# Optimization experiments

Measured on AMD Instinct MI355X. Metric: run time of the kernel, lower is better.

## Reference

```python
import jax, jax.numpy as jnp
import numpy as np

N, E, G = 400000, 2500000, 512
IN_F, H, C = 7, 32, 2
EPS = 1e-5


def setup_inputs() -> dict:
    key = jax.random.key(0)
    ks = jax.random.split(key, 12)
    x = jax.random.normal(ks[0], (N, IN_F), jnp.float32)
    edge_index = jax.random.randint(ks[1], (2, E), 0, N, dtype=jnp.int64)
    edge_attr = jax.random.uniform(ks[2], (E,), jnp.float32)
    batch = jnp.sort(jax.random.randint(ks[3], (N,), 0, G, dtype=jnp.int64))

    def lin(k, i, o):
        return (jax.random.normal(k, (i, o), jnp.float32) / np.sqrt(i)).astype(jnp.float32)

    params = dict(
        W0=lin(ks[4], IN_F, H), b0=jnp.zeros((H,), jnp.float32),
        W1=lin(ks[5], H, H),    b1=jnp.zeros((H,), jnp.float32),
        W2=lin(ks[6], H, H),    b2=jnp.zeros((H,), jnp.float32),
        W3=lin(ks[7], H, H),    b3=jnp.zeros((H,), jnp.float32),
        bn_g=jnp.ones((3, H), jnp.float32), bn_b=jnp.zeros((3, H), jnp.float32),
        Wm0=lin(ks[8], H, H),   bm0=jnp.zeros((H,), jnp.float32),
        bnm_g=jnp.ones((H,), jnp.float32), bnm_b=jnp.zeros((H,), jnp.float32),
        Wm1=lin(ks[9], H, C),   bm1=jnp.zeros((C,), jnp.float32),
    )
    return {"x": x, "edge_index": edge_index, "edge_attr": edge_attr, "batch": batch, **params}


def _batchnorm(h, g, b):
    # training-mode batch norm over the node/graph axis
    m = h.mean(axis=0)
    v = h.var(axis=0)
    return (h - m) * jax.lax.rsqrt(v + EPS) * g + b


def _gcn_forward(x, edge_index, edge_attr, batch,
                 W0, b0, W1, b1, W2, b2, W3, b3, bn_g, bn_b,
                 Wm0, bm0, bnm_g, bnm_b, Wm1, bm1):
    row, col = edge_index[0], edge_index[1]
    # add self-loops with weight 1 (GCNConv default), then symmetric normalization
    loop = jnp.arange(N, dtype=row.dtype)
    row = jnp.concatenate([row, loop])
    col = jnp.concatenate([col, loop])
    w = jnp.concatenate([edge_attr, jnp.ones((N,), edge_attr.dtype)])
    deg = jax.ops.segment_sum(w, col, num_segments=N)
    dinv = jnp.where(deg > 0, jax.lax.rsqrt(jnp.maximum(deg, EPS)), 0.0)
    norm = dinv[row] * w * dinv[col]  # [E+N]

    def conv(h, W, b):
        h = h @ W                                    # [N,H] dense transform
        msg = norm[:, None] * h[row]                 # gather + scale
        return jax.ops.segment_sum(msg, col, num_segments=N) + b  # scatter-add

    h = jax.nn.relu(_batchnorm(conv(x, W0, b0), bn_g[0], bn_b[0]))
    h = jax.nn.relu(_batchnorm(conv(h, W1, b1), bn_g[1], bn_b[1]))
    h = jax.nn.relu(_batchnorm(conv(h, W2, b2), bn_g[2], bn_b[2]))
    h = conv(h, W3, b3)                              # last GCN layer: no norm/act

    g = jax.ops.segment_sum(h, batch, num_segments=G)  # global_add_pool -> [G,H]
    g = jax.nn.relu(_batchnorm(g @ Wm0 + bm0, bnm_g, bnm_b))
    return g @ Wm1 + bm1                             # [G,C]


def reference(x, edge_index, edge_attr, batch,
              W0, b0, W1, b1, W2, b2, W3, b3, bn_g, bn_b,
              Wm0, bm0, bnm_g, bnm_b, Wm1, bm1):
    return _gcn_forward(x, edge_index, edge_attr, batch,
                        W0, b0, W1, b1, W2, b2, W3, b3, bn_g, bn_b,
                        Wm0, bm0, bnm_g, bnm_b, Wm1, bm1)
```

## Files before the change

### kernel.cpp

```cpp
#include <hip/hip_runtime.h>

#define TPB 256
#define RBITS 10
#define RSZ   1024
#define BMAX  512
#define CHUNK 4096
constexpr float EPSV = 1e-5f;

__device__ __forceinline__ float bf2f(unsigned short u) {
  return __uint_as_float((unsigned)u << 16);
}
__device__ __forceinline__ unsigned short f2bf(float f) {
  unsigned u = __float_as_uint(f);
  return (unsigned short)((u + 0x7fffu + ((u >> 16) & 1u)) >> 16);
}


__global__ void k_bcnt(const int* __restrict__ col, int* __restrict__ bcnt, int E, int B) {
  __shared__ int h[BMAX];
  const int tid = threadIdx.x;
  for (int i = tid; i < B; i += TPB) h[i] = 0;
  __syncthreads();
  const int e0 = blockIdx.x * CHUNK;
  for (int k = tid; k < CHUNK; k += TPB) {
    int i = e0 + k;
    if (i < E) atomicAdd(&h[col[i] >> RBITS], 1);
  }
  __syncthreads();
  for (int i = tid; i < B; i += TPB)
    if (h[i]) atomicAdd(&bcnt[i], h[i]);
}

__global__ void k_bscan(const int* __restrict__ bcnt, int* __restrict__ bbase,
                        int* __restrict__ bcur, int B, int E) {
  __shared__ int red[BMAX];
  const int tid = threadIdx.x;
  int v = (tid < B) ? bcnt[tid] : 0;
  red[tid] = v;
  __syncthreads();
  for (int off = 1; off < BMAX; off <<= 1) {
    int u = (tid >= off) ? red[tid - off] : 0;
    __syncthreads();
    red[tid] += u;
    __syncthreads();
  }
  int excl = red[tid] - v;
  if (tid < B) { bbase[tid] = excl; bcur[tid] = excl; }
  if (tid == 0) bbase[B] = E;
}

__global__ void k_binfill(const int* __restrict__ row, const int* __restrict__ col,
                          const float* __restrict__ w, int* __restrict__ bcur,
                          uint2* __restrict__ buck, int E, int B) {
  __shared__ int h[BMAX], base[BMAX], cur[BMAX];
  const int tid = threadIdx.x;
  for (int i = tid; i < B; i += TPB) { h[i] = 0; cur[i] = 0; }
  __syncthreads();
  const int e0 = blockIdx.x * CHUNK;
  for (int k = tid; k < CHUNK; k += TPB) {
    int i = e0 + k;
    if (i < E) atomicAdd(&h[col[i] >> RBITS], 1);
  }
  __syncthreads();
  for (int i = tid; i < B; i += TPB)
    base[i] = h[i] ? atomicAdd(&bcur[i], h[i]) : 0;
  __syncthreads();
  for (int k = tid; k < CHUNK; k += TPB) {
    int i = e0 + k;
    if (i >= E) continue;
    int c = col[i];
    int b = c >> RBITS;
    int pos = base[b] + atomicAdd(&cur[b], 1);
    unsigned lc = (unsigned)(c & (RSZ - 1));
    buck[pos] = make_uint2((unsigned)row[i] | (lc << 19), __float_as_uint(w[i]));
  }
}

__global__ __launch_bounds__(256) void k_bucket(const uint2* __restrict__ buck,
                                                const int* __restrict__ bbase,
                                                int* __restrict__ ptr, float* __restrict__ dinv,
                                                uint2* __restrict__ pk, int N, int E) {
  __shared__ int cnt[RSZ];
  __shared__ float wsum[RSZ];
  __shared__ int lofs[RSZ];
  __shared__ int red[256];
  const int bk = blockIdx.x, tid = threadIdx.x;
  const int n0 = bk << RBITS;
  const int nloc = min(RSZ, N - n0);
  for (int i = tid; i < RSZ; i += 256) { cnt[i] = 0; wsum[i] = 0.f; }
  __syncthreads();
  const int e0 = bbase[bk], e1 = bbase[bk + 1];
  for (int i = e0 + tid; i < e1; i += 256) {
    uint2 e = buck[i];
    int lc = e.x >> 19;
    atomicAdd(&cnt[lc], 1);
    atomicAdd(&wsum[lc], __uint_as_float(e.y));
  }
  __syncthreads();
  int a = cnt[tid * 4], b = cnt[tid * 4 + 1], c = cnt[tid * 4 + 2], d = cnt[tid * 4 + 3];
  int l1 = a, l2 = a + b, l3 = a + b + c, s = a + b + c + d;
  red[tid] = s;
  __syncthreads();
  for (int off = 1; off < 256; off <<= 1) {
    int u = (tid >= off) ? red[tid - off] : 0;
    __syncthreads();
    red[tid] += u;
    __syncthreads();
  }
  int tb = red[tid] - s;
  lofs[tid * 4] = tb; lofs[tid * 4 + 1] = tb + l1;
  lofs[tid * 4 + 2] = tb + l2; lofs[tid * 4 + 3] = tb + l3;
  __syncthreads();
  for (int i = tid; i < nloc; i += 256) {
    ptr[n0 + i] = e0 + lofs[i];
    dinv[n0 + i] = rsqrtf(1.0f + wsum[i]);
  }
  for (int i = tid; i < RSZ; i += 256) cnt[i] = 0;
  __syncthreads();
  for (int i = e0 + tid; i < e1; i += 256) {
    uint2 e = buck[i];
    int lc = e.x >> 19;
    int pos = e0 + lofs[lc] + atomicAdd(&cnt[lc], 1);
    pk[pos] = make_uint2(e.x & 524287u, e.y);
  }
  if (bk == 0 && tid == 0) ptr[N] = E;
}

__global__ void k_nrmcsr(uint2* __restrict__ pk, const int* __restrict__ ptr,
                         const float* __restrict__ dinv, int N) {
  int i = blockIdx.x * blockDim.x + threadIdx.x;
  if (i >= N) return;
  int p0 = ptr[i], p1 = ptr[i + 1];
  float dvc = dinv[i];
  for (int p = p0; p < p1; ++p) {
    uint2 e = pk[p];
    pk[p].y = __float_as_uint(dinv[e.x] * __uint_as_float(e.y) * dvc);
  }
}


__global__ void k_transform0(const float* __restrict__ in, const float* __restrict__ W,
                             unsigned short* __restrict__ t, int N) {
  __shared__ float Ws[7 * 32];
  __shared__ float hs[8 * 7];
  const int tid = threadIdx.x;
  const int n0 = blockIdx.x * 8;
  if (tid < 7 * 32) Ws[tid] = W[tid];
  if (tid < 8 * 7) {
    int node = n0 + tid / 7;
    hs[tid] = (node < N) ? in[n0 * 7 + tid] : 0.0f;
  }
  __syncthreads();
  const int j = tid >> 5, c = tid & 31;
  const int node = n0 + j;
  if (node < N) {
    float acc = 0.0f;
#pragma unroll
    for (int k = 0; k < 7; ++k) acc += hs[j * 7 + k] * Ws[k * 32 + c];
    t[(size_t)node * 32 + c] = f2bf(acc);
  }
}

__global__ void k_transform(const unsigned short* __restrict__ in, const float* __restrict__ W,
                            const float* __restrict__ gstats, const float* __restrict__ gamma,
                            const float* __restrict__ beta, float invN,
                            unsigned short* __restrict__ t, int N) {
  __shared__ float Ws[32 * 32];
  __shared__ float hs[8 * 32];
  __shared__ float ssb[64];
  const int tid = threadIdx.x;
  const int n0 = blockIdx.x * 8;
  for (int k = tid; k < 1024; k += TPB) Ws[k] = W[k];
  if (tid < 32) {
    float m = gstats[tid] * invN;
    float v = gstats[32 + tid] * invN - m * m;
    float sc = gamma[tid] * rsqrtf(v + EPSV);
    ssb[tid] = sc;
    ssb[32 + tid] = beta[tid] - m * sc;
  }
  __syncthreads();
  {
    int node = n0 + (tid >> 5);
    int c = tid & 31;
    float v = 0.0f;
    if (node < N) {
      v = bf2f(in[(size_t)n0 * 32 + tid]);
      v = fmaxf(v * ssb[c] + ssb[32 + c], 0.0f);
    }
    hs[tid] = v;
  }
  __syncthreads();
  const int j = tid >> 5, c = tid & 31;
  const int node = n0 + j;
  if (node < N) {
    float acc = 0.0f;
#pragma unroll
    for (int k = 0; k < 32; ++k) acc += hs[j * 32 + k] * Ws[k * 32 + c];
    t[(size_t)node * 32 + c] = f2bf(acc);
  }
}


__device__ __forceinline__ void fma8(float* acc, uint4 v, float wt) {
  acc[0] += wt * __uint_as_float(v.x << 16);
  acc[1] += wt * __uint_as_float(v.x & 0xffff0000u);
  acc[2] += wt * __uint_as_float(v.y << 16);
  acc[3] += wt * __uint_as_float(v.y & 0xffff0000u);
  acc[4] += wt * __uint_as_float(v.z << 16);
  acc[5] += wt * __uint_as_float(v.z & 0xffff0000u);
  acc[6] += wt * __uint_as_float(v.w << 16);
  acc[7] += wt * __uint_as_float(v.w & 0xffff0000u);
}

__global__ __launch_bounds__(256, 4) void k_gather(
    const uint2* __restrict__ pk, const int* __restrict__ ptr,
    const float* __restrict__ dinv, const uint4* __restrict__ t4,
    uint4* __restrict__ out4, int N) {
  const int n = blockIdx.x * 256 + threadIdx.x;
  if (n >= N) return;
  const int p0 = ptr[n], p1 = ptr[n + 1];
  const float dvn = dinv[n];
  float acc[32];
  {
    const float wt = dvn * dvn;
    const size_t rb = (size_t)n * 4;
    uint4 A = t4[rb], B = t4[rb + 1], C = t4[rb + 2], D = t4[rb + 3];
#pragma unroll
    for (int k = 0; k < 32; ++k) acc[k] = 0.f;
    fma8(acc, A, wt); fma8(acc + 8, B, wt); fma8(acc + 16, C, wt); fma8(acc + 24, D, wt);
  }
  for (int p = p0; p < p1; ++p) {
    uint2 e = pk[p];
    const float wt = __uint_as_float(e.y);
    const size_t rb = (size_t)e.x * 4;
    uint4 A = t4[rb], B = t4[rb + 1], C = t4[rb + 2], D = t4[rb + 3];
    fma8(acc, A, wt); fma8(acc + 8, B, wt); fma8(acc + 16, C, wt); fma8(acc + 24, D, wt);
  }
  const size_t ob = (size_t)n * 4;
#pragma unroll
  for (int q = 0; q < 4; ++q) {
    uint4 o;
    o.x = (unsigned)f2bf(acc[q * 8 + 0]) | ((unsigned)f2bf(acc[q * 8 + 1]) << 16);
    o.y = (unsigned)f2bf(acc[q * 8 + 2]) | ((unsigned)f2bf(acc[q * 8 + 3]) << 16);
    o.z = (unsigned)f2bf(acc[q * 8 + 4]) | ((unsigned)f2bf(acc[q * 8 + 5]) << 16);
    o.w = (unsigned)f2bf(acc[q * 8 + 6]) | ((unsigned)f2bf(acc[q * 8 + 7]) << 16);
    out4[ob + q] = o;
  }
}


__global__ void k_stats(const uint4* __restrict__ x4, float* __restrict__ gstats, int nquads) {
  __shared__ float ls[64];
  const int tid = threadIdx.x;
  if (tid < 64) ls[tid] = 0.f;
  __syncthreads();
  const int q = tid & 3;
  float s[8], sq[8];
#pragma unroll
  for (int k = 0; k < 8; ++k) { s[k] = 0.f; sq[k] = 0.f; }
  for (int idx = blockIdx.x * TPB + tid; idx < nquads; idx += gridDim.x * TPB) {
    uint4 v = x4[idx];
    float f0 = __uint_as_float(v.x << 16), f1 = __uint_as_float(v.x & 0xffff0000u);
    float f2 = __uint_as_float(v.y << 16), f3 = __uint_as_float(v.y & 0xffff0000u);
    float f4 = __uint_as_float(v.z << 16), f5 = __uint_as_float(v.z & 0xffff0000u);
    float f6 = __uint_as_float(v.w << 16), f7 = __uint_as_float(v.w & 0xffff0000u);
    s[0] += f0; sq[0] += f0 * f0;  s[1] += f1; sq[1] += f1 * f1;
    s[2] += f2; sq[2] += f2 * f2;  s[3] += f3; sq[3] += f3 * f3;
    s[4] += f4; sq[4] += f4 * f4;  s[5] += f5; sq[5] += f5 * f5;
    s[6] += f6; sq[6] += f6 * f6;  s[7] += f7; sq[7] += f7 * f7;
  }
#pragma unroll
  for (int k = 0; k < 8; ++k) {
    int c = q * 8 + k;
    atomicAdd(&ls[c], s[k]);
    atomicAdd(&ls[32 + c], sq[k]);
  }
  __syncthreads();
  if (tid < 64) unsafeAtomicAdd(&gstats[tid], ls[tid]);
}


__global__ void k_pool(const unsigned short* __restrict__ h, const int* __restrict__ batch,
                       const float* __restrict__ b3, float* __restrict__ pool, int N) {
  __shared__ float red[TPB];
  int g = blockIdx.x, tid = threadIdx.x;
  int lo = 0, hi = N;
  while (lo < hi) { int mid = (lo + hi) >> 1; if (batch[mid] < g) lo = mid + 1; else hi = mid; }
  int start = lo;
  hi = N;
  while (lo < hi) { int mid = (lo + hi) >> 1; if (batch[mid] < g + 1) lo = mid + 1; else hi = mid; }
  int end = lo;
  int j = tid >> 5, c = tid & 31;
  float acc = 0.f;
  for (int i = start + j; i < end; i += 8) acc += bf2f(h[(size_t)i * 32 + c]);
  red[tid] = acc;
  __syncthreads();
  for (int off = 128; off >= 32; off >>= 1) {
    if (tid < off) red[tid] += red[tid + off];
    __syncthreads();
  }
  if (tid < 32) pool[g * 32 + tid] = red[tid] + (float)(end - start) * b3[tid];
}


__global__ void k_mlpz(const float* __restrict__ pool, const float* __restrict__ Wm0,
                       const float* __restrict__ bm0, float* __restrict__ z,
                       float* __restrict__ mstats) {
  __shared__ float Ws[32 * 32];
  __shared__ float ps[8 * 32];
  __shared__ float ls[TPB], lq[TPB];
  const int tid = threadIdx.x;
  const int g0 = blockIdx.x * 8;
  for (int k = tid; k < 1024; k += TPB) Ws[k] = Wm0[k];
  if (tid < 256) ps[tid] = pool[g0 * 32 + tid];
  __syncthreads();
  const int j = tid >> 5, c = tid & 31;
  float acc = bm0[c];
#pragma unroll
  for (int k = 0; k < 32; ++k) acc += ps[j * 32 + k] * Ws[k * 32 + c];
  z[(g0 + j) * 32 + c] = acc;
  ls[tid] = acc;
  lq[tid] = acc * acc;
  __syncthreads();
  for (int off = 128; off >= 32; off >>= 1) {
    if (tid < off) { ls[tid] += ls[tid + off]; lq[tid] += lq[tid + off]; }
    __syncthreads();
  }
  if (tid < 32) {
    unsafeAtomicAdd(&mstats[tid], ls[tid]);
    unsafeAtomicAdd(&mstats[32 + tid], lq[tid]);
  }
}

__global__ void k_mlpfin(const float* __restrict__ z, const float* __restrict__ mstats,
                         const float* __restrict__ bng, const float* __restrict__ bnb,
                         const float* __restrict__ Wm1, const float* __restrict__ bm1,
                         float* __restrict__ out) {
  __shared__ float sc[32], sh[32], w1[64];
  const int tid = threadIdx.x;
  if (tid < 32) {
    float m = mstats[tid] * (1.0f / 512.0f);
    float v = mstats[32 + tid] * (1.0f / 512.0f) - m * m;
    float s = bng[tid] * rsqrtf(v + EPSV);
    sc[tid] = s;
    sh[tid] = bnb[tid] - m * s;
  }
  if (tid < 64) w1[tid] = Wm1[tid];
  __syncthreads();
  const int g = tid >> 1, o = tid & 1;
  float acc = bm1[o];
#pragma unroll
  for (int c = 0; c < 32; ++c) {
    float hc = fmaxf(z[g * 32 + c] * sc[c] + sh[c], 0.f);
    acc += hc * w1[c * 2 + o];
  }
  out[tid] = acc;
}


extern "C" void kernel_launch(void* const* d_in, const int* in_sizes, int n_in,
                              void* d_out, int out_size, void* d_ws, size_t ws_size,
                              hipStream_t stream) {
  const float* x     = (const float*)d_in[0];
  const int*   ei    = (const int*)d_in[1];
  const float* ea    = (const float*)d_in[2];
  const int*   batch = (const int*)d_in[3];
  const float* W0    = (const float*)d_in[4];
  const float* W1    = (const float*)d_in[6];
  const float* W2    = (const float*)d_in[8];
  const float* W3    = (const float*)d_in[10];
  const float* b3    = (const float*)d_in[11];
  const float* bng   = (const float*)d_in[12];
  const float* bnb   = (const float*)d_in[13];
  const float* Wm0   = (const float*)d_in[14];
  const float* bm0   = (const float*)d_in[15];
  const float* bnmg  = (const float*)d_in[16];
  const float* bnmb  = (const float*)d_in[17];
  const float* Wm1   = (const float*)d_in[18];
  const float* bm1   = (const float*)d_in[19];
  float* out = (float*)d_out;

  const int N = in_sizes[3];
  const int E = in_sizes[2];
  const int* row = ei;
  const int* col = ei + E;
  const int B = (N + RSZ - 1) >> RBITS;

  char* wsb = (char*)d_ws;
  auto alloc = [&](size_t bytes) { char* p = wsb; wsb += (bytes + 255) & ~size_t(255); return p; };
  int*   bcnt  = (int*)alloc((size_t)(BMAX + 1) * 4);
  int*   bbase = (int*)alloc((size_t)(BMAX + 1) * 4);
  int*   bcur  = (int*)alloc((size_t)BMAX * 4);
  int*   ptr   = (int*)alloc((size_t)(N + 1) * 4);
  uint2* buck  = (uint2*)alloc((size_t)E * 8);
  uint2* pk    = (uint2*)alloc((size_t)E * 8);
  float* dinv  = (float*)alloc((size_t)N * 4);
  unsigned short* B0 = (unsigned short*)alloc((size_t)N * 32 * 2);
  unsigned short* B1 = (unsigned short*)alloc((size_t)N * 32 * 2);
  float* stats = (float*)alloc(4 * 64 * 4);
  float* pool  = (float*)alloc(512 * 32 * 4);
  float* zbuf  = (float*)alloc(512 * 32 * 4);

  hipMemsetAsync(bcnt, 0, (size_t)(BMAX + 1) * 4, stream);
  hipMemsetAsync(stats, 0, 4 * 64 * 4, stream);

  const int nb_n = (N + TPB - 1) / TPB;
  const int nb_c = (E + CHUNK - 1) / CHUNK;
  const int nb_t = (N + 7) / 8;
  const int nb_g = (N + 255) / 256;
  const int nquads = N * 4;
  const float invN = 1.0f / (float)N;
  float* mstats = stats + 192;

  k_bcnt<<<nb_c, TPB, 0, stream>>>(col, bcnt, E, B);
  k_bscan<<<1, BMAX, 0, stream>>>(bcnt, bbase, bcur, B, E);
  k_binfill<<<nb_c, TPB, 0, stream>>>(row, col, ea, bcur, buck, E, B);
  k_bucket<<<B, 256, 0, stream>>>(buck, bbase, ptr, dinv, pk, N, E);
  k_nrmcsr<<<nb_n, TPB, 0, stream>>>(pk, ptr, dinv, N);

  k_transform0<<<nb_t, TPB, 0, stream>>>(x, W0, B0, N);
  k_gather<<<nb_g, 256, 0, stream>>>(pk, ptr, dinv, (const uint4*)B0, (uint4*)B1, N);
  k_stats<<<1024, TPB, 0, stream>>>((const uint4*)B1, stats, nquads);

  k_transform<<<nb_t, TPB, 0, stream>>>(B1, W1, stats, bng, bnb, invN, B0, N);
  k_gather<<<nb_g, 256, 0, stream>>>(pk, ptr, dinv, (const uint4*)B0, (uint4*)B1, N);
  k_stats<<<1024, TPB, 0, stream>>>((const uint4*)B1, stats + 64, nquads);

  k_transform<<<nb_t, TPB, 0, stream>>>(B1, W2, stats + 64, bng + 32, bnb + 32, invN, B0, N);
  k_gather<<<nb_g, 256, 0, stream>>>(pk, ptr, dinv, (const uint4*)B0, (uint4*)B1, N);
  k_stats<<<1024, TPB, 0, stream>>>((const uint4*)B1, stats + 128, nquads);

  k_transform<<<nb_t, TPB, 0, stream>>>(B1, W3, stats + 128, bng + 64, bnb + 64, invN, B0, N);
  k_gather<<<nb_g, 256, 0, stream>>>(pk, ptr, dinv, (const uint4*)B0, (uint4*)B1, N);

  k_pool<<<512, TPB, 0, stream>>>(B1, batch, b3, pool, N);
  k_mlpz<<<64, TPB, 0, stream>>>(pool, Wm0, bm0, zbuf, mstats);
  k_mlpfin<<<1, 1024, 0, stream>>>(zbuf, mstats, bnmg, bnmb, Wm1, bm1, out);
}
```

Before: 874.7 us.

## Fuse BN stats into gather, edge-parallel normalization, retile transform and pool

Folds the per-destination degree scaling into the bucket kernel and replaces the per-node CSR normalization loop with an edge-parallel kernel. It removes the separate stats kernels by accumulating sums and squares inside the gather via shared-memory atomics. The transform now handles 32 nodes per block with 4 outputs per thread and vectorized bf16 loads, and pooling uses uint4 loads with a tree reduction. The gather stats path adds heavy LDS atomic contention, with 64 atomics per thread on shared addresses.

```diff
diff --git a/kernel.cpp b/kernel.cpp
--- a/kernel.cpp
+++ b/kernel.cpp
@@ -121,20 +121,17 @@
     uint2 e = buck[i];
     int lc = e.x >> 19;
     int pos = e0 + lofs[lc] + atomicAdd(&cnt[lc], 1);
-    pk[pos] = make_uint2(e.x & 524287u, e.y);
+    float wdc = __uint_as_float(e.y) * rsqrtf(1.0f + wsum[lc]);
+    pk[pos] = make_uint2(e.x & 524287u, __float_as_uint(wdc));
   }
   if (bk == 0 && tid == 0) ptr[N] = E;
 }
 
-__global__ void k_nrmcsr(uint2* __restrict__ pk, const int* __restrict__ ptr,
-                         const float* __restrict__ dinv, int N) {
-  int i = blockIdx.x * blockDim.x + threadIdx.x;
-  if (i >= N) return;
-  int p0 = ptr[i], p1 = ptr[i + 1];
-  float dvc = dinv[i];
-  for (int p = p0; p < p1; ++p) {
-    uint2 e = pk[p];
-    pk[p].y = __float_as_uint(dinv[e.x] * __uint_as_float(e.y) * dvc);
+__global__ void k_nrme(uint2* __restrict__ pk, const float* __restrict__ dinv, int E) {
+  int e = blockIdx.x * blockDim.x + threadIdx.x;
+  if (e < E) {
+    uint2 v = pk[e];
+    pk[e].y = __float_as_uint(__uint_as_float(v.y) * dinv[v.x]);
   }
 }
 
@@ -161,16 +158,17 @@
   }
 }
 
-__global__ void k_transform(const unsigned short* __restrict__ in, const float* __restrict__ W,
-                            const float* __restrict__ gstats, const float* __restrict__ gamma,
-                            const float* __restrict__ beta, float invN,
-                            unsigned short* __restrict__ t, int N) {
-  __shared__ float Ws[32 * 32];
-  __shared__ float hs[8 * 32];
+__global__ __launch_bounds__(256) void k_transform(
+    const uint4* __restrict__ in4, const float* __restrict__ W,
+    const float* __restrict__ gstats, const float* __restrict__ gamma,
+    const float* __restrict__ beta, float invN, uint2* __restrict__ t2, int N) {
+  __shared__ float Ws[1024];
+  __shared__ float hs[32 * 33];
   __shared__ float ssb[64];
   const int tid = threadIdx.x;
-  const int n0 = blockIdx.x * 8;
-  for (int k = tid; k < 1024; k += TPB) Ws[k] = W[k];
+  const int n0 = blockIdx.x * 32;
+#pragma unroll
+  for (int k = 0; k < 4; ++k) Ws[k * 256 + tid] = W[k * 256 + tid];
   if (tid < 32) {
     float m = gstats[tid] * invN;
     float v = gstats[32 + tid] * invN - m * m;
@@ -179,24 +177,39 @@
     ssb[32 + tid] = beta[tid] - m * sc;
   }
   __syncthreads();
-  {
-    int node = n0 + (tid >> 5);
-    int c = tid & 31;
-    float v = 0.0f;
-    if (node < N) {
-      v = bf2f(in[(size_t)n0 * 32 + tid]);
-      v = fmaxf(v * ssb[c] + ssb[32 + c], 0.0f);
-    }
-    hs[tid] = v;
-  }
-  __syncthreads();
-  const int j = tid >> 5, c = tid & 31;
+  if (tid < 128) {
+    const int r = tid >> 2, q = tid & 3;
+    const int node = n0 + r;
+    uint4 v = make_uint4(0, 0, 0, 0);
+    if (node < N) v = in4[(size_t)node * 4 + q];
+    float* h = &hs[r * 33 + q * 8];
+    const float* sc = &ssb[q * 8];
+    const float* sh = &ssb[32 + q * 8];
+    h[0] = fmaxf(__uint_as_float(v.x << 16) * sc[0] + sh[0], 0.f);
+    h[1] = fmaxf(__uint_as_float(v.x & 0xffff0000u) * sc[1] + sh[1], 0.f);
+    h[2] = fmaxf(__uint_as_float(v.y << 16) * sc[2] + sh[2], 0.f);
+    h[3] = fmaxf(__uint_as_float(v.y & 0xffff0000u) * sc[3] + sh[3], 0.f);
+    h[4] = fmaxf(__uint_as_float(v.z << 16) * sc[4] + sh[4], 0.f);
+    h[5] = fmaxf(__uint_as_float(v.z & 0xffff0000u) * sc[5] + sh[5], 0.f);
+    h[6] = fmaxf(__uint_as_float(v.w << 16) * sc[6] + sh[6], 0.f);
+    h[7] = fmaxf(__uint_as_float(v.w & 0xffff0000u) * sc[7] + sh[7], 0.f);
+  }
+  __syncthreads();
+  const int j = tid >> 3;
+  const int c0 = (tid & 7) * 4;
   const int node = n0 + j;
   if (node < N) {
-    float acc = 0.0f;
-#pragma unroll
-    for (int k = 0; k < 32; ++k) acc += hs[j * 32 + k] * Ws[k * 32 + c];
-    t[(size_t)node * 32 + c] = f2bf(acc);
+    float a0 = 0.f, a1 = 0.f, a2 = 0.f, a3 = 0.f;
+#pragma unroll
+    for (int k = 0; k < 32; ++k) {
+      float v = hs[j * 33 + k];
+      const float* w = &Ws[k * 32 + c0];
+      a0 += v * w[0]; a1 += v * w[1]; a2 += v * w[2]; a3 += v * w[3];
+    }
+    uint2 o;
+    o.x = (unsigned)f2bf(a0) | ((unsigned)f2bf(a1) << 16);
+    o.y = (unsigned)f2bf(a2) | ((unsigned)f2bf(a3) << 16);
+    t2[(size_t)node * 8 + (tid & 7)] = o;
   }
 }
 
@@ -212,91 +225,95 @@
   acc[7] += wt * __uint_as_float(v.w & 0xffff0000u);
 }
 
+template <bool STATS>
 __global__ __launch_bounds__(256, 4) void k_gather(
     const uint2* __restrict__ pk, const int* __restrict__ ptr,
     const float* __restrict__ dinv, const uint4* __restrict__ t4,
-    uint4* __restrict__ out4, int N) {
-  const int n = blockIdx.x * 256 + threadIdx.x;
-  if (n >= N) return;
-  const int p0 = ptr[n], p1 = ptr[n + 1];
-  const float dvn = dinv[n];
+    uint4* __restrict__ out4, float* __restrict__ gstats, int N) {
+  __shared__ float ls[64];
+  const int tid = threadIdx.x;
+  if (STATS) {
+    if (tid < 64) ls[tid] = 0.f;
+    __syncthreads();
+  }
+  const int n = blockIdx.x * 256 + tid;
+  const bool act = n < N;
   float acc[32];
-  {
-    const float wt = dvn * dvn;
-    const size_t rb = (size_t)n * 4;
-    uint4 A = t4[rb], B = t4[rb + 1], C = t4[rb + 2], D = t4[rb + 3];
-#pragma unroll
-    for (int k = 0; k < 32; ++k) acc[k] = 0.f;
-    fma8(acc, A, wt); fma8(acc + 8, B, wt); fma8(acc + 16, C, wt); fma8(acc + 24, D, wt);
-  }
-  for (int p = p0; p < p1; ++p) {
-    uint2 e = pk[p];
-    const float wt = __uint_as_float(e.y);
-    const size_t rb = (size_t)e.x * 4;
-    uint4 A = t4[rb], B = t4[rb + 1], C = t4[rb + 2], D = t4[rb + 3];
-    fma8(acc, A, wt); fma8(acc + 8, B, wt); fma8(acc + 16, C, wt); fma8(acc + 24, D, wt);
-  }
-  const size_t ob = (size_t)n * 4;
-#pragma unroll
-  for (int q = 0; q < 4; ++q) {
-    uint4 o;
-    o.x = (unsigned)f2bf(acc[q * 8 + 0]) | ((unsigned)f2bf(acc[q * 8 + 1]) << 16);
-    o.y = (unsigned)f2bf(acc[q * 8 + 2]) | ((unsigned)f2bf(acc[q * 8 + 3]) << 16);
-    o.z = (unsigned)f2bf(acc[q * 8 + 4]) | ((unsigned)f2bf(acc[q * 8 + 5]) << 16);
-    o.w = (unsigned)f2bf(acc[q * 8 + 6]) | ((unsigned)f2bf(acc[q * 8 + 7]) << 16);
-    out4[ob + q] = o;
-  }
-}
-
-
-__global__ void k_stats(const uint4* __restrict__ x4, float* __restrict__ gstats, int nquads) {
-  __shared__ float ls[64];
-  const int tid = threadIdx.x;
-  if (tid < 64) ls[tid] = 0.f;
-  __syncthreads();
-  const int q = tid & 3;
-  float s[8], sq[8];
-#pragma unroll
-  for (int k = 0; k < 8; ++k) { s[k] = 0.f; sq[k] = 0.f; }
-  for (int idx = blockIdx.x * TPB + tid; idx < nquads; idx += gridDim.x * TPB) {
-    uint4 v = x4[idx];
-    float f0 = __uint_as_float(v.x << 16), f1 = __uint_as_float(v.x & 0xffff0000u);
-    float f2 = __uint_as_float(v.y << 16), f3 = __uint_as_float(v.y & 0xffff0000u);
-    float f4 = __uint_as_float(v.z << 16), f5 = __uint_as_float(v.z & 0xffff0000u);
-    float f6 = __uint_as_float(v.w << 16), f7 = __uint_as_float(v.w & 0xffff0000u);
-    s[0] += f0; sq[0] += f0 * f0;  s[1] += f1; sq[1] += f1 * f1;
-    s[2] += f2; sq[2] += f2 * f2;  s[3] += f3; sq[3] += f3 * f3;
-    s[4] += f4; sq[4] += f4 * f4;  s[5] += f5; sq[5] += f5 * f5;
-    s[6] += f6; sq[6] += f6 * f6;  s[7] += f7; sq[7] += f7 * f7;
-  }
-#pragma unroll
-  for (int k = 0; k < 8; ++k) {
-    int c = q * 8 + k;
-    atomicAdd(&ls[c], s[k]);
-    atomicAdd(&ls[32 + c], sq[k]);
-  }
-  __syncthreads();
-  if (tid < 64) unsafeAtomicAdd(&gstats[tid], ls[tid]);
-}
-
-
-__global__ void k_pool(const unsigned short* __restrict__ h, const int* __restrict__ batch,
-                       const float* __restrict__ b3, float* __restrict__ pool, int N) {
-  __shared__ float red[TPB];
-  int g = blockIdx.x, tid = threadIdx.x;
+#pragma unroll
+  for (int k = 0; k < 32; ++k) acc[k] = 0.f;
+  if (act) {
+    const int p0 = ptr[n], p1 = ptr[n + 1];
+    const float dvn = dinv[n];
+    {
+      const float wt = dvn * dvn;
+      const size_t rb = (size_t)n * 4;
+      uint4 A = t4[rb], B = t4[rb + 1], C = t4[rb + 2], D = t4[rb + 3];
+      fma8(acc, A, wt); fma8(acc + 8, B, wt); fma8(acc + 16, C, wt); fma8(acc + 24, D, wt);
+    }
+    for (int p = p0; p < p1; ++p) {
+      uint2 e = pk[p];
+      const float wt = __uint_as_float(e.y);
+      const size_t rb = (size_t)e.x * 4;
+      uint4 A = t4[rb], B = t4[rb + 1], C = t4[rb + 2], D = t4[rb + 3];
+      fma8(acc, A, wt); fma8(acc + 8, B, wt); fma8(acc + 16, C, wt); fma8(acc + 24, D, wt);
+    }
+    const size_t ob = (size_t)n * 4;
+#pragma unroll
+    for (int q = 0; q < 4; ++q) {
+      uint4 o;
+      o.x = (unsigned)f2bf(acc[q * 8 + 0]) | ((unsigned)f2bf(acc[q * 8 + 1]) << 16);
+      o.y = (unsigned)f2bf(acc[q * 8 + 2]) | ((unsigned)f2bf(acc[q * 8 + 3]) << 16);
+      o.z = (unsigned)f2bf(acc[q * 8 + 4]) | ((unsigned)f2bf(acc[q * 8 + 5]) << 16);
+      o.w = (unsigned)f2bf(acc[q * 8 + 6]) | ((unsigned)f2bf(acc[q * 8 + 7]) << 16);
+      out4[ob + q] = o;
+    }
+  }
+  if (STATS) {
+    if (act) {
+#pragma unroll
+      for (int k = 0; k < 32; ++k) {
+        atomicAdd(&ls[k], acc[k]);
+        atomicAdd(&ls[32 + k], acc[k] * acc[k]);
+      }
+    }
+    __syncthreads();
+    if (tid < 64) unsafeAtomicAdd(&gstats[tid], ls[tid]);
+  }
+}
+
+
+__global__ __launch_bounds__(256) void k_pool(
+    const uint4* __restrict__ h4, const int* __restrict__ batch,
+    const float* __restrict__ b3, float* __restrict__ pool, int N) {
+  __shared__ float red[64 * 33];
+  const int g = blockIdx.x, tid = threadIdx.x;
   int lo = 0, hi = N;
   while (lo < hi) { int mid = (lo + hi) >> 1; if (batch[mid] < g) lo = mid + 1; else hi = mid; }
-  int start = lo;
+  const int start = lo;
   hi = N;
   while (lo < hi) { int mid = (lo + hi) >> 1; if (batch[mid] < g + 1) lo = mid + 1; else hi = mid; }
-  int end = lo;
-  int j = tid >> 5, c = tid & 31;
-  float acc = 0.f;
-  for (int i = start + j; i < end; i += 8) acc += bf2f(h[(size_t)i * 32 + c]);
-  red[tid] = acc;
-  __syncthreads();
-  for (int off = 128; off >= 32; off >>= 1) {
-    if (tid < off) red[tid] += red[tid + off];
+  const int end = lo;
+  const int j = tid >> 2, q = tid & 3;
+  float a[8];
+#pragma unroll
+  for (int k = 0; k < 8; ++k) a[k] = 0.f;
+  for (int i = start + j; i < end; i += 64) {
+    uint4 v = h4[(size_t)i * 4 + q];
+    a[0] += __uint_as_float(v.x << 16); a[1] += __uint_as_float(v.x & 0xffff0000u);
+    a[2] += __uint_as_float(v.y << 16); a[3] += __uint_as_float(v.y & 0xffff0000u);
+    a[4] += __uint_as_float(v.z << 16); a[5] += __uint_as_float(v.z & 0xffff0000u);
+    a[6] += __uint_as_float(v.w << 16); a[7] += __uint_as_float(v.w & 0xffff0000u);
+  }
+  float* r = &red[j * 33 + ((q * 8) >= 16 ? (q * 8) + 0 : q * 8)];
+#pragma unroll
+  for (int k = 0; k < 8; ++k) red[j * 33 + q * 8 + k] = a[k];
+  __syncthreads();
+  for (int off = 32; off >= 1; off >>= 1) {
+    if (j < off) {
+#pragma unroll
+      for (int k = 0; k < 8; ++k)
+        red[j * 33 + q * 8 + k] += red[(j + off) * 33 + q * 8 + k];
+    }
     __syncthreads();
   }
   if (tid < 32) pool[g * 32 + tid] = red[tid] + (float)(end - start) * b3[tid];
@@ -404,11 +421,11 @@
   hipMemsetAsync(bcnt, 0, (size_t)(BMAX + 1) * 4, stream);
   hipMemsetAsync(stats, 0, 4 * 64 * 4, stream);
 
-  const int nb_n = (N + TPB - 1) / TPB;
   const int nb_c = (E + CHUNK - 1) / CHUNK;
-  const int nb_t = (N + 7) / 8;
+  const int nb_e = (E + 255) / 256;
+  const int nb_t0 = (N + 7) / 8;
+  const int nb_t = (N + 31) / 32;
   const int nb_g = (N + 255) / 256;
-  const int nquads = N * 4;
   const float invN = 1.0f / (float)N;
   float* mstats = stats + 192;
 
@@ -416,24 +433,28 @@
   k_bscan<<<1, BMAX, 0, stream>>>(bcnt, bbase, bcur, B, E);
   k_binfill<<<nb_c, TPB, 0, stream>>>(row, col, ea, bcur, buck, E, B);
   k_bucket<<<B, 256, 0, stream>>>(buck, bbase, ptr, dinv, pk, N, E);
-  k_nrmcsr<<<nb_n, TPB, 0, stream>>>(pk, ptr, dinv, N);
-
-  k_transform0<<<nb_t, TPB, 0, stream>>>(x, W0, B0, N);
-  k_gather<<<nb_g, 256, 0, stream>>>(pk, ptr, dinv, (const uint4*)B0, (uint4*)B1, N);
-  k_stats<<<1024, TPB, 0, stream>>>((const uint4*)B1, stats, nquads);
-
-  k_transform<<<nb_t, TPB, 0, stream>>>(B1, W1, stats, bng, bnb, invN, B0, N);
-  k_gather<<<nb_g, 256, 0, stream>>>(pk, ptr, dinv, (const uint4*)B0, (uint4*)B1, N);
-  k_stats<<<1024, TPB, 0, stream>>>((const uint4*)B1, stats + 64, nquads);
-
-  k_transform<<<nb_t, TPB, 0, stream>>>(B1, W2, stats + 64, bng + 32, bnb + 32, invN, B0, N);
-  k_gather<<<nb_g, 256, 0, stream>>>(pk, ptr, dinv, (const uint4*)B0, (uint4*)B1, N);
-  k_stats<<<1024, TPB, 0, stream>>>((const uint4*)B1, stats + 128, nquads);
-
-  k_transform<<<nb_t, TPB, 0, stream>>>(B1, W3, stats + 128, bng + 64, bnb + 64, invN, B0, N);
-  k_gather<<<nb_g, 256, 0, stream>>>(pk, ptr, dinv, (const uint4*)B0, (uint4*)B1, N);
-
-  k_pool<<<512, TPB, 0, stream>>>(B1, batch, b3, pool, N);
+  k_nrme<<<nb_e, 256, 0, stream>>>(pk, dinv, E);
+
+  k_transform0<<<nb_t0, TPB, 0, stream>>>(x, W0, B0, N);
+  k_gather<true><<<nb_g, 256, 0, stream>>>(pk, ptr, dinv, (const uint4*)B0,
+                                           (uint4*)B1, stats, N);
+
+  k_transform<<<nb_t, 256, 0, stream>>>((const uint4*)B1, W1, stats, bng, bnb, invN,
+                                        (uint2*)B0, N);
+  k_gather<true><<<nb_g, 256, 0, stream>>>(pk, ptr, dinv, (const uint4*)B0,
+                                           (uint4*)B1, stats + 64, N);
+
+  k_transform<<<nb_t, 256, 0, stream>>>((const uint4*)B1, W2, stats + 64, bng + 32, bnb + 32,
+                                        invN, (uint2*)B0, N);
+  k_gather<true><<<nb_g, 256, 0, stream>>>(pk, ptr, dinv, (const uint4*)B0,
+                                           (uint4*)B1, stats + 128, N);
+
+  k_transform<<<nb_t, 256, 0, stream>>>((const uint4*)B1, W3, stats + 128, bng + 64, bnb + 64,
+                                        invN, (uint2*)B0, N);
+  k_gather<false><<<nb_g, 256, 0, stream>>>(pk, ptr, dinv, (const uint4*)B0,
+                                            (uint4*)B1, nullptr, N);
+
+  k_pool<<<512, 256, 0, stream>>>((const uint4*)B1, batch, b3, pool, N);
   k_mlpz<<<64, TPB, 0, stream>>>(pool, Wm0, bm0, zbuf, mstats);
   k_mlpfin<<<1, 1024, 0, stream>>>(zbuf, mstats, bnmg, bnmb, Wm1, bm1, out);
 }
```

New measurement: 1.371 ms. +56.7%, slower.
